# Kernel tuning notes

Hardware: AMD Instinct MI355X
Metric: run time of the kernel (lower is better)

The kernel has to match this reference:

```python
import jax, jax.numpy as jnp
import numpy as np
import math

B, L, D, H, FF = 8, 1024, 1024, 16, 4096
DT = D // H  # d_tensor per head
EPS = 1e-12


def _layernorm(x, gamma, beta):
    # Faithful: unbiased std (ddof=1), divide by (std + eps)
    mean = jnp.mean(x, axis=-1, keepdims=True)
    std = jnp.std(x, axis=-1, keepdims=True, ddof=1)
    return gamma * ((x - mean) / (std + EPS)) + beta


def setup_inputs() -> dict:
    key = jax.random.key(0)
    ks = jax.random.split(key, 16)
    sc = 1.0 / math.sqrt(D)
    inp = {
        "x": jax.random.normal(ks[0], (B, L, D), jnp.float32),
        "s_mask": jnp.ones((B, 1, L, L), jnp.int32),
        "wq": jax.random.normal(ks[1], (D, D), jnp.float32) * sc,
        "bq": jnp.zeros((D,), jnp.float32),
        "wk": jax.random.normal(ks[2], (D, D), jnp.float32) * sc,
        "bk": jnp.zeros((D,), jnp.float32),
        "wv": jax.random.normal(ks[3], (D, D), jnp.float32) * sc,
        "bv": jnp.zeros((D,), jnp.float32),
        "wc": jax.random.normal(ks[4], (D, D), jnp.float32) * sc,
        "bc": jnp.zeros((D,), jnp.float32),
        "g1": jnp.ones((D,), jnp.float32),
        "be1": jnp.zeros((D,), jnp.float32),
        "w1": jax.random.normal(ks[5], (D, FF), jnp.float32) * sc,
        "b1": jnp.zeros((FF,), jnp.float32),
        "w2": jax.random.normal(ks[6], (FF, D), jnp.float32) / math.sqrt(FF),
        "b2": jnp.zeros((D,), jnp.float32),
        "g2": jnp.ones((D,), jnp.float32),
        "be2": jnp.zeros((D,), jnp.float32),
    }
    return inp


def reference(x, s_mask, wq, bq, wk, bk, wv, bv, wc, bc, g1, be1, w1, b1, w2, b2, g2, be2):
    _x = x
    q = x @ wq + bq
    k = x @ wk + bk
    v = x @ wv + bv
    # Faithful quirk: split() is a VIEW/reshape [B,L,D] -> [B,H,L,DT], not a transpose-based head split.
    q = q.reshape(B, H, L, DT)
    k = k.reshape(B, H, L, DT)
    v = v.reshape(B, H, L, DT)
    # Faithful quirk: k_t is a reshape to [B,H,DT,L], not a transpose.
    k_t = k.reshape(B, H, DT, L)
    score = jnp.einsum('bhld,bhdm->bhlm', q, k_t) / math.sqrt(DT)
    # Faithful quirk: masked_fill value is -1e-12 (not -inf)
    score = jnp.where(s_mask == 0, jnp.float32(-EPS), score)
    # Faithful quirk: nn.Softmax() with dim=None on 4D tensor -> softmax over dim=1 (head axis)
    score = jax.nn.softmax(score, axis=1)
    out = jnp.einsum('bhlm,bhmd->bhld', score, v)
    out = out.reshape(B, L, D)
    out = out @ wc + bc
    x = _layernorm(out + _x, g1, be1)
    # dropout1: identity at inference
    _x = x
    h = jax.nn.relu(x @ w1 + b1)  # FFN dropout also identity at inference
    h = h @ w2 + b2
    x = _layernorm(h + _x, g2, be2)
    return x
```

## Files before the change

kernel.cpp:

```cpp
#include <hip/hip_runtime.h>
#include <stdint.h>

typedef unsigned short u16;
typedef __attribute__((ext_vector_type(8))) short sx8;
typedef __attribute__((ext_vector_type(4))) float fx4;

__device__ __forceinline__ float bf2f(u16 u) {
    union { unsigned i; float f; } v; v.i = ((unsigned)u) << 16; return v.f;
}
__device__ __forceinline__ u16 f2bf(float f) {
    union { float f; unsigned i; } v; v.f = f;
    return (u16)((v.i + 0x7FFFu + ((v.i >> 16) & 1u)) >> 16);
}
#define MFMA(a, b, c) __builtin_amdgcn_mfma_f32_16x16x32_bf16((a), (b), (c), 0, 0, 0)

#define GLDS(gp, lp) \
    __builtin_amdgcn_global_load_lds((const __attribute__((address_space(1))) void*)(gp), \
                                     (__attribute__((address_space(3))) void*)(lp), 16, 0, 0)

template<int BN>
__global__ __launch_bounds__(256) void gemm_bt(
    const u16* __restrict__ A, long sA, int ldA,
    const u16* __restrict__ BT, long sBT, int ldBT,
    u16* __restrict__ C, long sC, int ldC,
    int K,
    const u16* __restrict__ bias, int bz,
    const void* __restrict__ resid, int residF32, long rofs,
    float scale, int relu)
{
    constexpr int BK = 32;
    constexpr int TM = 4;
    constexpr int TN = BN / 32;
    constexpr int AI = 2;
    constexpr int BI = BN / 64;

    __shared__ __align__(16) u16 As[128 * BK];
    __shared__ __align__(16) u16 Bs[BN * BK];

    const int tid  = threadIdx.x;
    const int w    = tid >> 6;
    const int lane = tid & 63;
    const int quad = lane >> 4;
    const int n16  = lane & 15;
    const int wrow = w >> 1, wcol = w & 1;
    const int m0 = blockIdx.y * 128, n0 = blockIdx.x * BN;
    const long z = blockIdx.z;
    A  += z * sA;
    BT += z * sBT;
    C  += z * sC;

    fx4 acc[TM][TN] = {};

    for (int k0 = 0; k0 < K; k0 += BK) {
        #pragma unroll
        for (int i = 0; i < AI; ++i) {
            unsigned base = (unsigned)(w * AI + i) * 1024u;
            unsigned off  = base + (unsigned)lane * 16u;
            unsigned row  = off >> 6;
            unsigned col  = (off & 63u) >> 1;
            GLDS(A + (long)(m0 + row) * ldA + k0 + col, (char*)As + base);
        }
        #pragma unroll
        for (int i = 0; i < BI; ++i) {
            unsigned base = (unsigned)(w * BI + i) * 1024u;
            unsigned off  = base + (unsigned)lane * 16u;
            unsigned row  = off >> 6;
            unsigned col  = (off & 63u) >> 1;
            GLDS(BT + (long)(n0 + row) * ldBT + k0 + col, (char*)Bs + base);
        }
        __syncthreads();

        sx8 af[TM], bfr[TN];
        #pragma unroll
        for (int r = 0; r < TM; ++r)
            af[r] = *(const sx8*)&As[(wrow * 64 + r * 16 + n16) * BK + quad * 8];
        #pragma unroll
        for (int c = 0; c < TN; ++c)
            bfr[c] = *(const sx8*)&Bs[(wcol * (TN * 16) + c * 16 + n16) * BK + quad * 8];
        #pragma unroll
        for (int r = 0; r < TM; ++r)
            #pragma unroll
            for (int c = 0; c < TN; ++c)
                acc[r][c] = MFMA(af[r], bfr[c], acc[r][c]);
        __syncthreads();
    }

    #pragma unroll
    for (int r = 0; r < TM; ++r) {
        int row = m0 + wrow * 64 + r * 16 + quad * 4;
        #pragma unroll
        for (int c = 0; c < TN; ++c) {
            int col = n0 + wcol * (TN * 16) + c * 16 + n16;
            float bv = bias ? bf2f(bias[bz * (int)z + col]) : 0.f;
            #pragma unroll
            for (int g = 0; g < 4; ++g) {
                long idx = (long)(row + g) * ldC + col;
                float xv = acc[r][c][g] * scale + bv;
                if (resid)
                    xv += residF32 ? ((const float*)resid)[rofs + idx]
                                   : bf2f(((const u16*)resid)[rofs + idx]);
                if (relu) xv = fmaxf(xv, 0.f);
                C[idx] = f2bf(xv);
            }
        }
    }
}

__global__ __launch_bounds__(256, 4) void attn_fused(
    const u16* __restrict__ qb, const u16* __restrict__ kt,
    const u16* __restrict__ vt, const int* __restrict__ mask,
    u16* __restrict__ p0, u16* __restrict__ p1)
{
    constexpr int MC = 64;
    constexpr int LM = MC + 8;
    constexpr int SH = 16 * LM;
    __shared__ __align__(16) u16 Ss[16 * SH];

    const int tid = threadIdx.x, w = tid >> 6, lane = tid & 63;
    const int quad = lane >> 4, n16 = lane & 15;
    const int l0 = blockIdx.x * 16;
    const long bo = (long)blockIdx.y * 1048576;
    const int mbase = blockIdx.z * 512;
    u16* __restrict__ po = blockIdx.z ? p1 : p0;

    sx8 qf[4][2];
    #pragma unroll
    for (int i = 0; i < 4; ++i) {
        const u16* qp = qb + bo + (w * 4 + i) * 65536 + (l0 + n16) * 64 + quad * 8;
        qf[i][0] = *(const sx8*)qp;
        qf[i][1] = *(const sx8*)(qp + 32);
    }

    fx4 of[4][4] = {};

    for (int mt = 0; mt < 8; ++mt) {
        const int m0 = mbase + mt * MC;
        #pragma unroll
        for (int i = 0; i < 4; ++i) {
            const int h = w * 4 + i;
            const u16* kp = kt + bo + h * 65536 + (long)m0 * 64;
            #pragma unroll
            for (int nt = 0; nt < 4; ++nt) {
                const u16* kr = kp + (nt * 16 + n16) * 64 + quad * 8;
                fx4 s = {};
                s = MFMA(*(const sx8*)kr,        qf[i][0], s);
                s = MFMA(*(const sx8*)(kr + 32), qf[i][1], s);
                uint2 pk;
                pk.x = (unsigned)f2bf(s[0] * 0.125f) | ((unsigned)f2bf(s[1] * 0.125f) << 16);
                pk.y = (unsigned)f2bf(s[2] * 0.125f) | ((unsigned)f2bf(s[3] * 0.125f) << 16);
                *(uint2*)&Ss[h * SH + n16 * LM + nt * 16 + quad * 4] = pk;
            }
        }
        __syncthreads();
        #pragma unroll
        for (int j = 0; j < 2; ++j) {
            const int p = tid + 256 * j;
            const int l = p >> 5, mp = (p & 31) * 2;
            const int2 mk = *(const int2*)&mask[bo + (long)(l0 + l) * 1024 + m0 + mp];
            u16* col = &Ss[l * LM + mp];
            float v0[16], v1[16], mx0 = -1e30f, mx1 = -1e30f;
            #pragma unroll
            for (int h = 0; h < 16; ++h) {
                unsigned pr = *(const unsigned*)&col[h * SH];
                float a = (mk.x == 0) ? -1e-12f : bf2f((u16)(pr & 0xffff));
                float b = (mk.y == 0) ? -1e-12f : bf2f((u16)(pr >> 16));
                v0[h] = a; v1[h] = b;
                mx0 = fmaxf(mx0, a); mx1 = fmaxf(mx1, b);
            }
            float s0 = 0.f, s1 = 0.f;
            #pragma unroll
            for (int h = 0; h < 16; ++h) {
                v0[h] = __expf(v0[h] - mx0); s0 += v0[h];
                v1[h] = __expf(v1[h] - mx1); s1 += v1[h];
            }
            const float i0 = 1.f / s0, i1 = 1.f / s1;
            #pragma unroll
            for (int h = 0; h < 16; ++h)
                *(unsigned*)&col[h * SH] =
                    (unsigned)f2bf(v0[h] * i0) | ((unsigned)f2bf(v1[h] * i1) << 16);
        }
        __syncthreads();
        #pragma unroll
        for (int i = 0; i < 4; ++i) {
            const int h = w * 4 + i;
            const u16* sp = &Ss[h * SH + n16 * LM];
            sx8 a0 = *(const sx8*)(sp + quad * 8);
            sx8 a1 = *(const sx8*)(sp + 32 + quad * 8);
            const u16* vp = vt + bo + h * 65536 + (long)n16 * 1024 + m0 + quad * 8;
            #pragma unroll
            for (int dt = 0; dt < 4; ++dt) {
                of[i][dt] = MFMA(a0, *(const sx8*)(vp + dt * 16384),      of[i][dt]);
                of[i][dt] = MFMA(a1, *(const sx8*)(vp + dt * 16384 + 32), of[i][dt]);
            }
        }
        __syncthreads();
    }

    #pragma unroll
    for (int i = 0; i < 4; ++i) {
        const int h = w * 4 + i;
        #pragma unroll
        for (int dt = 0; dt < 4; ++dt)
            #pragma unroll
            for (int r = 0; r < 4; ++r)
                po[bo + h * 65536 + (long)(l0 + quad * 4 + r) * 64 + dt * 16 + n16]
                    = f2bf(of[i][dt][r]);
    }
}

__global__ __launch_bounds__(256) void add_bf(
    const u16* __restrict__ a, u16* __restrict__ b)
{
    long i = ((long)blockIdx.x * 256 + threadIdx.x) * 8;
    uint4 x = *(const uint4*)(a + i);
    uint4 y = *(const uint4*)(b + i);
    uint4 r;
    unsigned* xp = (unsigned*)&x; unsigned* yp = (unsigned*)&y; unsigned* rp = (unsigned*)&r;
    #pragma unroll
    for (int k = 0; k < 4; ++k) {
        float lo = bf2f((u16)(xp[k] & 0xffff)) + bf2f((u16)(yp[k] & 0xffff));
        float hi = bf2f((u16)(xp[k] >> 16))    + bf2f((u16)(yp[k] >> 16));
        rp[k] = (unsigned)f2bf(lo) | ((unsigned)f2bf(hi) << 16);
    }
    *(uint4*)(b + i) = r;
}

__global__ __launch_bounds__(256) void convert_f2b(
    const float* __restrict__ in, u16* __restrict__ out)
{
    long i = ((long)blockIdx.x * 256 + threadIdx.x) * 4;
    fx4 v = *(const fx4*)(in + i);
    uint2 o;
    o.x = (unsigned)f2bf(v[0]) | ((unsigned)f2bf(v[1]) << 16);
    o.y = (unsigned)f2bf(v[2]) | ((unsigned)f2bf(v[3]) << 16);
    *(uint2*)(out + i) = o;
}

__global__ __launch_bounds__(256) void transpose_f2b(
    const float* __restrict__ in, u16* __restrict__ out, int R, int C)
{
    __shared__ float t[32][33];
    int c0 = blockIdx.x * 32, r0 = blockIdx.y * 32;
    int tx = threadIdx.x & 31, ty = threadIdx.x >> 5;
    #pragma unroll
    for (int i = 0; i < 4; ++i)
        t[ty + i * 8][tx] = in[(long)(r0 + ty + i * 8) * C + c0 + tx];
    __syncthreads();
    #pragma unroll
    for (int i = 0; i < 4; ++i)
        out[(long)(c0 + ty + i * 8) * R + r0 + tx] = f2bf(t[tx][ty + i * 8]);
}

__global__ __launch_bounds__(256) void transpose_bf(
    const u16* __restrict__ in, u16* __restrict__ out, int R, int C)
{
    __shared__ u16 t[32][33];
    long zoff = (long)blockIdx.z * (long)R * (long)C;
    in += zoff; out += zoff;
    int c0 = blockIdx.x * 32, r0 = blockIdx.y * 32;
    int tx = threadIdx.x & 31, ty = threadIdx.x >> 5;
    #pragma unroll
    for (int i = 0; i < 4; ++i)
        t[ty + i * 8][tx] = in[(long)(r0 + ty + i * 8) * C + c0 + tx];
    __syncthreads();
    #pragma unroll
    for (int i = 0; i < 4; ++i)
        out[(long)(c0 + ty + i * 8) * R + r0 + tx] = t[tx][ty + i * 8];
}

__global__ __launch_bounds__(256) void pack_bias(
    const float* bq, const float* bk, const float* bv, const float* bc,
    const float* b1, const float* b2, u16* __restrict__ out)
{
    int i = blockIdx.x * 256 + threadIdx.x;
    float v;
    if      (i < 1024) v = bq[i];
    else if (i < 2048) v = bk[i - 1024];
    else if (i < 3072) v = bv[i - 2048];
    else if (i < 4096) v = bc[i - 3072];
    else if (i < 8192) v = b1[i - 4096];
    else               v = b2[i - 8192];
    out[i] = f2bf(v);
}

__global__ __launch_bounds__(256) void layernorm_row(
    const u16* __restrict__ in, const float* __restrict__ g,
    const float* __restrict__ be, void* __restrict__ out, int outF32)
{
    int wave = threadIdx.x >> 6, lane = threadIdx.x & 63;
    long row = (long)blockIdx.x * 4 + wave;
    const u16* p = in + row * 1024 + lane * 16;

    float x[16];
    uint4 a = ((const uint4*)p)[0], b = ((const uint4*)p)[1];
    {
        unsigned u;
        u = a.x; x[0] = bf2f(u & 0xffff);  x[1] = bf2f(u >> 16);
        u = a.y; x[2] = bf2f(u & 0xffff);  x[3] = bf2f(u >> 16);
        u = a.z; x[4] = bf2f(u & 0xffff);  x[5] = bf2f(u >> 16);
        u = a.w; x[6] = bf2f(u & 0xffff);  x[7] = bf2f(u >> 16);
        u = b.x; x[8] = bf2f(u & 0xffff);  x[9] = bf2f(u >> 16);
        u = b.y; x[10] = bf2f(u & 0xffff); x[11] = bf2f(u >> 16);
        u = b.z; x[12] = bf2f(u & 0xffff); x[13] = bf2f(u >> 16);
        u = b.w; x[14] = bf2f(u & 0xffff); x[15] = bf2f(u >> 16);
    }
    float s = 0.f, ss = 0.f;
    #pragma unroll
    for (int i = 0; i < 16; ++i) { s += x[i]; ss += x[i] * x[i]; }
    #pragma unroll
    for (int o = 32; o >= 1; o >>= 1) { s += __shfl_down(s, o); ss += __shfl_down(ss, o); }
    s = __shfl(s, 0); ss = __shfl(ss, 0);
    float mean = s * (1.f / 1024.f);
    float var  = fmaxf((ss - 1024.f * mean * mean) * (1.f / 1023.f), 0.f);
    float rinv = 1.f / (sqrtf(var) + 1e-12f);

    int col = lane * 16;
    if (outF32) {
        float* ov = (float*)out + row * 1024 + col;
        #pragma unroll
        for (int i = 0; i < 16; ++i)
            ov[i] = g[col + i] * ((x[i] - mean) * rinv) + be[col + i];
    } else {
        u16* ov = (u16*)out + row * 1024 + col;
        #pragma unroll
        for (int i = 0; i < 16; ++i)
            ov[i] = f2bf(g[col + i] * ((x[i] - mean) * rinv) + be[col + i]);
    }
}

extern "C" void kernel_launch(void* const* d_in, const int* in_sizes, int n_in,
                              void* d_out, int out_size, void* d_ws, size_t ws_size,
                              hipStream_t stream)
{
    const float* xf  = (const float*)d_in[0];
    const int* mask  = (const int*)d_in[1];
    const float* wq = (const float*)d_in[2];  const float* bq = (const float*)d_in[3];
    const float* wk = (const float*)d_in[4];  const float* bk = (const float*)d_in[5];
    const float* wv = (const float*)d_in[6];  const float* bv = (const float*)d_in[7];
    const float* wc = (const float*)d_in[8];  const float* bc = (const float*)d_in[9];
    const float* g1 = (const float*)d_in[10]; const float* be1 = (const float*)d_in[11];
    const float* w1 = (const float*)d_in[12]; const float* b1 = (const float*)d_in[13];
    const float* w2 = (const float*)d_in[14]; const float* b2 = (const float*)d_in[15];
    const float* g2 = (const float*)d_in[16]; const float* be2 = (const float*)d_in[17];

    char* ws = (char*)d_ws;
    const long MB = 1 << 20;
    u16* xb    = (u16*)(ws + 0 * MB);
    u16* wqkvT = (u16*)(ws + 16 * MB);
    u16* wcT   = (u16*)(ws + 22 * MB);
    u16* qb    = (u16*)(ws + 24 * MB);
    u16* kb    = (u16*)(ws + 40 * MB);
    u16* vb    = (u16*)(ws + 56 * MB);
    u16* kt    = (u16*)(ws + 72 * MB);
    u16* vt    = (u16*)(ws + 40 * MB);
    u16* biasp = (u16*)(ws + 96 * MB);
    u16* p0   = xb;
    u16* p1   = vb;
    u16* ao   = p1;
    u16* t0   = qb;
    u16* fh   = kb;
    u16* w1T  = (u16*)(ws + 72 * MB);
    u16* w2T  = (u16*)(ws + 80 * MB);
    u16* pre2 = (u16*)(ws + 88 * MB);

    dim3 blk(256);
    const long M1 = 1048576;

    convert_f2b<<<dim3(8192), blk, 0, stream>>>(xf, xb);
    transpose_f2b<<<dim3(32, 32), blk, 0, stream>>>(wq, wqkvT, 1024, 1024);
    transpose_f2b<<<dim3(32, 32), blk, 0, stream>>>(wk, wqkvT + M1, 1024, 1024);
    transpose_f2b<<<dim3(32, 32), blk, 0, stream>>>(wv, wqkvT + 2 * M1, 1024, 1024);
    transpose_f2b<<<dim3(32, 32), blk, 0, stream>>>(wc, wcT, 1024, 1024);
    pack_bias<<<dim3(36), blk, 0, stream>>>(bq, bk, bv, bc, b1, b2, biasp);

    gemm_bt<128><<<dim3(8, 64, 3), blk, 0, stream>>>(
        xb, 0, 1024, wqkvT, M1, 1024, qb, 8 * M1, 1024, 1024,
        biasp, 1024, nullptr, 0, 0, 1.f, 0);

    transpose_bf<<<dim3(32, 2, 128), blk, 0, stream>>>(kb, kt, 64, 1024);

    transpose_bf<<<dim3(2, 32, 128), blk, 0, stream>>>(vb, vt, 1024, 64);
    attn_fused<<<dim3(64, 8, 2), blk, 0, stream>>>(qb, kt, vt, mask, p0, p1);
    add_bf<<<dim3(4096), blk, 0, stream>>>(p0, p1);

    gemm_bt<128><<<dim3(8, 64, 1), blk, 0, stream>>>(
        ao, 0, 1024, wcT, 0, 1024, t0, 0, 1024, 1024,
        biasp + 3072, 0, xf, 1, 0, 1.f, 0);
    layernorm_row<<<dim3(2048), blk, 0, stream>>>(t0, g1, be1, t0, 0);

    transpose_f2b<<<dim3(128, 32), blk, 0, stream>>>(w1, w1T, 1024, 4096);
    transpose_f2b<<<dim3(32, 128), blk, 0, stream>>>(w2, w2T, 4096, 1024);

    for (int c = 0; c < 2; ++c) {
        long r0 = (long)c * 4096 * 1024;
        gemm_bt<128><<<dim3(32, 32, 1), blk, 0, stream>>>(
            t0 + r0, 0, 1024, w1T, 0, 1024, fh, 0, 4096, 1024,
            biasp + 4096, 0, nullptr, 0, 0, 1.f, 1);
        gemm_bt<64><<<dim3(16, 32, 1), blk, 0, stream>>>(
            fh, 0, 4096, w2T, 0, 4096, pre2, 0, 1024, 4096,
            biasp + 8192, 0, t0 + r0, 0, 0, 1.f, 0);
        layernorm_row<<<dim3(1024), blk, 0, stream>>>(
            pre2, g2, be2, (float*)d_out + r0, 1);
    }
}
```

Baseline: 944.6 us.

## Use 512-thread attention blocks with two heads per wave and XCD-aware block mapping

The fused attention kernel now launches 512-thread blocks, so each of the eight waves handles two heads instead of four. This halves the per-wave Q fragments and output accumulators to lower register pressure and raise occupancy. The launch becomes a 1D grid whose block index is remapped so neighbouring work lands on the same XCD, aiming for better L2 reuse of K/V. The softmax now keeps packed bf16 scores and recomputes exp instead of holding float arrays, trading extra transcendental work for fewer registers.

```diff
diff --git a/kernel.cpp b/kernel.cpp
--- a/kernel.cpp
+++ b/kernel.cpp
@@ -106,7 +106,7 @@
     }
 }
 
-__global__ __launch_bounds__(256, 4) void attn_fused(
+__global__ __launch_bounds__(512, 6) void attn_fused(
     const u16* __restrict__ qb, const u16* __restrict__ kt,
     const u16* __restrict__ vt, const int* __restrict__ mask,
     u16* __restrict__ p0, u16* __restrict__ p1)
@@ -118,26 +118,29 @@
 
     const int tid = threadIdx.x, w = tid >> 6, lane = tid & 63;
     const int quad = lane >> 4, n16 = lane & 15;
-    const int l0 = blockIdx.x * 16;
-    const long bo = (long)blockIdx.y * 1048576;
-    const int mbase = blockIdx.z * 512;
-    u16* __restrict__ po = blockIdx.z ? p1 : p0;
-
-    sx8 qf[4][2];
-    #pragma unroll
-    for (int i = 0; i < 4; ++i) {
-        const u16* qp = qb + bo + (w * 4 + i) * 65536 + (l0 + n16) * 64 + quad * 8;
+
+    const int wg = ((blockIdx.x & 7) << 7) + (blockIdx.x >> 3);
+    const int l0 = (wg & 63) * 16;
+    const long bo = (long)((wg >> 6) & 7) * 1048576;
+    const int zz = wg >> 9;
+    const int mbase = zz * 512;
+    u16* __restrict__ po = zz ? p1 : p0;
+
+    sx8 qf[2][2];
+    #pragma unroll
+    for (int i = 0; i < 2; ++i) {
+        const u16* qp = qb + bo + (w * 2 + i) * 65536 + (l0 + n16) * 64 + quad * 8;
         qf[i][0] = *(const sx8*)qp;
         qf[i][1] = *(const sx8*)(qp + 32);
     }
 
-    fx4 of[4][4] = {};
+    fx4 of[2][4] = {};
 
     for (int mt = 0; mt < 8; ++mt) {
         const int m0 = mbase + mt * MC;
         #pragma unroll
-        for (int i = 0; i < 4; ++i) {
-            const int h = w * 4 + i;
+        for (int i = 0; i < 2; ++i) {
+            const int h = w * 2 + i;
             const u16* kp = kt + bo + h * 65536 + (long)m0 * 64;
             #pragma unroll
             for (int nt = 0; nt < 4; ++nt) {
@@ -152,37 +155,41 @@
             }
         }
         __syncthreads();
-        #pragma unroll
-        for (int j = 0; j < 2; ++j) {
-            const int p = tid + 256 * j;
-            const int l = p >> 5, mp = (p & 31) * 2;
+        {
+            const int l = tid >> 5, mp = (tid & 31) * 2;
             const int2 mk = *(const int2*)&mask[bo + (long)(l0 + l) * 1024 + m0 + mp];
             u16* col = &Ss[l * LM + mp];
-            float v0[16], v1[16], mx0 = -1e30f, mx1 = -1e30f;
+            const unsigned negc = (unsigned)f2bf(-1e-12f);
+            unsigned pr[16];
+            float mx0 = -1e30f, mx1 = -1e30f;
             #pragma unroll
             for (int h = 0; h < 16; ++h) {
-                unsigned pr = *(const unsigned*)&col[h * SH];
-                float a = (mk.x == 0) ? -1e-12f : bf2f((u16)(pr & 0xffff));
-                float b = (mk.y == 0) ? -1e-12f : bf2f((u16)(pr >> 16));
-                v0[h] = a; v1[h] = b;
-                mx0 = fmaxf(mx0, a); mx1 = fmaxf(mx1, b);
+                unsigned t = *(const unsigned*)&col[h * SH];
+                unsigned lo = mk.x ? (t & 0xffffu) : negc;
+                unsigned hi = mk.y ? (t >> 16)     : negc;
+                pr[h] = lo | (hi << 16);
+                mx0 = fmaxf(mx0, bf2f((u16)lo));
+                mx1 = fmaxf(mx1, bf2f((u16)hi));
             }
             float s0 = 0.f, s1 = 0.f;
             #pragma unroll
             for (int h = 0; h < 16; ++h) {
-                v0[h] = __expf(v0[h] - mx0); s0 += v0[h];
-                v1[h] = __expf(v1[h] - mx1); s1 += v1[h];
+                s0 += __expf(bf2f((u16)(pr[h] & 0xffffu)) - mx0);
+                s1 += __expf(bf2f((u16)(pr[h] >> 16))     - mx1);
             }
             const float i0 = 1.f / s0, i1 = 1.f / s1;
             #pragma unroll
-            for (int h = 0; h < 16; ++h)
+            for (int h = 0; h < 16; ++h) {
+                float e0 = __expf(bf2f((u16)(pr[h] & 0xffffu)) - mx0) * i0;
+                float e1 = __expf(bf2f((u16)(pr[h] >> 16))     - mx1) * i1;
                 *(unsigned*)&col[h * SH] =
-                    (unsigned)f2bf(v0[h] * i0) | ((unsigned)f2bf(v1[h] * i1) << 16);
+                    (unsigned)f2bf(e0) | ((unsigned)f2bf(e1) << 16);
+            }
         }
         __syncthreads();
         #pragma unroll
-        for (int i = 0; i < 4; ++i) {
-            const int h = w * 4 + i;
+        for (int i = 0; i < 2; ++i) {
+            const int h = w * 2 + i;
             const u16* sp = &Ss[h * SH + n16 * LM];
             sx8 a0 = *(const sx8*)(sp + quad * 8);
             sx8 a1 = *(const sx8*)(sp + 32 + quad * 8);
@@ -197,8 +204,8 @@
     }
 
     #pragma unroll
-    for (int i = 0; i < 4; ++i) {
-        const int h = w * 4 + i;
+    for (int i = 0; i < 2; ++i) {
+        const int h = w * 2 + i;
         #pragma unroll
         for (int dt = 0; dt < 4; ++dt)
             #pragma unroll
@@ -380,7 +387,7 @@
     transpose_bf<<<dim3(32, 2, 128), blk, 0, stream>>>(kb, kt, 64, 1024);
 
     transpose_bf<<<dim3(2, 32, 128), blk, 0, stream>>>(vb, vt, 1024, 64);
-    attn_fused<<<dim3(64, 8, 2), blk, 0, stream>>>(qb, kt, vt, mask, p0, p1);
+    attn_fused<<<dim3(1024), dim3(512), 0, stream>>>(qb, kt, vt, mask, p0, p1);
     add_bf<<<dim3(4096), blk, 0, stream>>>(p0, p1);
 
     gemm_bt<128><<<dim3(8, 64, 1), blk, 0, stream>>>(
```

After: 975.8 us. +3.3%, slower.

## Remap workgroups for XCD locality and fold score scale into Q projection

Applied to the files above, without the earlier changes.

Adds an XCD-aware workgroup index remap to the GEMM and attention kernels, so that neighbouring tiles sharing A/B or K/V data land on the same chiplet's L2. It also folds the 1/sqrt(DT) score scale into the Q projection epilogue and the Q bias, which removes per-element multiplies in the attention score loop. The attention grid is flattened to 1D to allow the remap. The remap only applies when the tile count is a multiple of 8. Pre-scaling Q before bf16 rounding changes rounding only slightly, because 0.125 is a power of two.

```diff
diff --git a/kernel.cpp b/kernel.cpp
--- a/kernel.cpp
+++ b/kernel.cpp
@@ -26,7 +26,7 @@
     int K,
     const u16* __restrict__ bias, int bz,
     const void* __restrict__ resid, int residF32, long rofs,
-    float scale, int relu)
+    float scale, int scaleZ0, int relu)
 {
     constexpr int BK = 32;
     constexpr int TM = 4;
@@ -43,8 +43,20 @@
     const int quad = lane >> 4;
     const int n16  = lane & 15;
     const int wrow = w >> 1, wcol = w & 1;
-    const int m0 = blockIdx.y * 128, n0 = blockIdx.x * BN;
+
+    int bx = blockIdx.x, by = blockIdx.y;
+    {
+        int nxy = gridDim.x * gridDim.y;
+        if ((nxy & 7) == 0) {
+            int bid = by * gridDim.x + bx;
+            int wgs = (bid & 7) * (nxy >> 3) + (bid >> 3);
+            bx = wgs % gridDim.x;
+            by = wgs / gridDim.x;
+        }
+    }
+    const int m0 = by * 128, n0 = bx * BN;
     const long z = blockIdx.z;
+    const float es = (z == 0 || !scaleZ0) ? scale : 1.f;
     A  += z * sA;
     BT += z * sBT;
     C  += z * sC;
@@ -95,7 +107,7 @@
             #pragma unroll
             for (int g = 0; g < 4; ++g) {
                 long idx = (long)(row + g) * ldC + col;
-                float xv = acc[r][c][g] * scale + bv;
+                float xv = acc[r][c][g] * es + bv;
                 if (resid)
                     xv += residF32 ? ((const float*)resid)[rofs + idx]
                                    : bf2f(((const u16*)resid)[rofs + idx]);
@@ -118,10 +130,13 @@
 
     const int tid = threadIdx.x, w = tid >> 6, lane = tid & 63;
     const int quad = lane >> 4, n16 = lane & 15;
-    const int l0 = blockIdx.x * 16;
-    const long bo = (long)blockIdx.y * 1048576;
-    const int mbase = blockIdx.z * 512;
-    u16* __restrict__ po = blockIdx.z ? p1 : p0;
+
+    const int wg = ((blockIdx.x & 7) << 7) + (blockIdx.x >> 3);
+    const int l0 = (wg & 63) * 16;
+    const long bo = (long)((wg >> 6) & 7) * 1048576;
+    const int zz = wg >> 9;
+    const int mbase = zz * 512;
+    u16* __restrict__ po = zz ? p1 : p0;
 
     sx8 qf[4][2];
     #pragma unroll
@@ -146,8 +161,8 @@
                 s = MFMA(*(const sx8*)kr,        qf[i][0], s);
                 s = MFMA(*(const sx8*)(kr + 32), qf[i][1], s);
                 uint2 pk;
-                pk.x = (unsigned)f2bf(s[0] * 0.125f) | ((unsigned)f2bf(s[1] * 0.125f) << 16);
-                pk.y = (unsigned)f2bf(s[2] * 0.125f) | ((unsigned)f2bf(s[3] * 0.125f) << 16);
+                pk.x = (unsigned)f2bf(s[0]) | ((unsigned)f2bf(s[1]) << 16);
+                pk.y = (unsigned)f2bf(s[2]) | ((unsigned)f2bf(s[3]) << 16);
                 *(uint2*)&Ss[h * SH + n16 * LM + nt * 16 + quad * 4] = pk;
             }
         }
@@ -274,7 +289,7 @@
 {
     int i = blockIdx.x * 256 + threadIdx.x;
     float v;
-    if      (i < 1024) v = bq[i];
+    if      (i < 1024) v = bq[i] * 0.125f;
     else if (i < 2048) v = bk[i - 1024];
     else if (i < 3072) v = bv[i - 2048];
     else if (i < 4096) v = bc[i - 3072];
@@ -375,17 +390,17 @@
 
     gemm_bt<128><<<dim3(8, 64, 3), blk, 0, stream>>>(
         xb, 0, 1024, wqkvT, M1, 1024, qb, 8 * M1, 1024, 1024,
-        biasp, 1024, nullptr, 0, 0, 1.f, 0);
+        biasp, 1024, nullptr, 0, 0, 0.125f, 1, 0);
 
     transpose_bf<<<dim3(32, 2, 128), blk, 0, stream>>>(kb, kt, 64, 1024);
 
     transpose_bf<<<dim3(2, 32, 128), blk, 0, stream>>>(vb, vt, 1024, 64);
-    attn_fused<<<dim3(64, 8, 2), blk, 0, stream>>>(qb, kt, vt, mask, p0, p1);
+    attn_fused<<<dim3(1024), blk, 0, stream>>>(qb, kt, vt, mask, p0, p1);
     add_bf<<<dim3(4096), blk, 0, stream>>>(p0, p1);
 
     gemm_bt<128><<<dim3(8, 64, 1), blk, 0, stream>>>(
         ao, 0, 1024, wcT, 0, 1024, t0, 0, 1024, 1024,
-        biasp + 3072, 0, xf, 1, 0, 1.f, 0);
+        biasp + 3072, 0, xf, 1, 0, 1.f, 0, 0);
     layernorm_row<<<dim3(2048), blk, 0, stream>>>(t0, g1, be1, t0, 0);
 
     transpose_f2b<<<dim3(128, 32), blk, 0, stream>>>(w1, w1T, 1024, 4096);
@@ -395,10 +410,10 @@
         long r0 = (long)c * 4096 * 1024;
         gemm_bt<128><<<dim3(32, 32, 1), blk, 0, stream>>>(
             t0 + r0, 0, 1024, w1T, 0, 1024, fh, 0, 4096, 1024,
-            biasp + 4096, 0, nullptr, 0, 0, 1.f, 1);
+            biasp + 4096, 0, nullptr, 0, 0, 1.f, 0, 1);
         gemm_bt<64><<<dim3(16, 32, 1), blk, 0, stream>>>(
             fh, 0, 4096, w2T, 0, 4096, pre2, 0, 1024, 4096,
-            biasp + 8192, 0, t0 + r0, 0, 0, 1.f, 0);
+            biasp + 8192, 0, t0 + r0, 0, 0, 1.f, 0, 0);
         layernorm_row<<<dim3(1024), blk, 0, stream>>>(
             pre2, g2, be2, (float*)d_out + r0, 1);
     }
```

Result: no change. 934.3 us (-1.1%).
